# Optimization experiments

Measured on AMD Instinct MI355X. Metric: run time of the kernel, lower is better.

Reference implementation:

```python
import jax, jax.numpy as jnp
import numpy as np

D_MODEL = 768
D_STATE = 64
EXPAND = 2
D_INNER = EXPAND * D_MODEL
B, L = 2, 1024


def setup_inputs() -> dict:
    key = jax.random.key(0)
    ks = jax.random.split(key, 12)
    def xavier(k, shape):
        fan_in, fan_out = shape[0], shape[1]
        a = np.sqrt(6.0 / (fan_in + fan_out)).astype(np.float32)
        return jax.random.uniform(k, shape, jnp.float32, -a, a)
    x = jax.random.normal(ks[0], (B, L, D_MODEL), jnp.float32)
    W_in = xavier(ks[1], (D_MODEL, 2 * D_INNER))
    W_x = xavier(ks[2], (D_INNER, 2 * D_STATE + D_INNER))
    W_dt = xavier(ks[3], (D_STATE, D_INNER))
    b_dt = jax.random.uniform(ks[4], (D_INNER,), jnp.float32, -0.1, 0.1)
    A_log = jax.random.uniform(ks[5], (D_INNER, D_STATE), jnp.float32, -4.0, -1.0)
    Dp = 1.0 + 0.1 * jax.random.normal(ks[6], (D_INNER,), jnp.float32)
    W_out = xavier(ks[7], (D_INNER, D_MODEL))
    ln_g = jnp.ones((D_MODEL,), jnp.float32)
    ln_b = jnp.zeros((D_MODEL,), jnp.float32)
    return {"x": x, "W_in": W_in, "W_x": W_x, "W_dt": W_dt, "b_dt": b_dt,
            "A_log": A_log, "Dp": Dp, "W_out": W_out, "ln_g": ln_g, "ln_b": ln_b}


def _s6_forward(x, W_in, W_x, W_dt, b_dt, A_log, Dp, W_out, ln_g, ln_b):
    residual = x
    xr = x @ W_in                                    # (B,L,2*d_inner)
    xs, res = xr[..., :D_INNER], xr[..., D_INNER:]
    xs = jax.nn.silu(xs)
    # selective scan parameters
    x_dbl = xs @ W_x                                 # (B,L,2*d_state+d_inner)
    B_sel = x_dbl[..., :D_STATE]                     # (B,L,d_state)
    delta_in = x_dbl[..., D_STATE:2 * D_STATE]       # (B,L,d_state)
    C_sel = x_dbl[..., 2 * D_STATE:]                 # (B,L,d_inner)
    delta = jax.nn.softplus(delta_in @ W_dt + b_dt)  # (B,L,d_inner)
    delta = jnp.minimum(delta, 10.0)
    A = -jnp.exp(A_log.astype(jnp.float32))          # (d_inner,d_state)

    def step(h, inp):
        x_t, d_t, B_t, C_t = inp                     # (B,di) (B,di) (B,ds) (B,di)
        dA = jnp.exp(d_t[:, :, None] * A[None])      # (B,di,ds)
        dB = d_t[:, :, None] * B_t[:, None, :]       # (B,di,ds)
        h = dA * h + dB * x_t[:, :, None]
        y_t = C_t * jnp.sum(h, axis=-1)              # (B,di): sum(C[...,None]*h,-1)
        return h, y_t

    h0 = jnp.zeros((x.shape[0], D_INNER, D_STATE), xs.dtype)
    time_major = lambda a: jnp.swapaxes(a, 0, 1)
    _, ys = jax.lax.scan(step, h0, (time_major(xs), time_major(delta),
                                    time_major(B_sel), time_major(C_sel)))
    y = jnp.swapaxes(ys, 0, 1)                       # (B,L,d_inner)
    y = y + xs * Dp
    y = y * jax.nn.silu(res)
    out = y @ W_out + residual
    mu = jnp.mean(out, axis=-1, keepdims=True)
    var = jnp.var(out, axis=-1, keepdims=True)
    return (out - mu) * jax.lax.rsqrt(var + 1e-5) * ln_g + ln_b


def reference(x, W_in, W_x, W_dt, b_dt, A_log, Dp, W_out, ln_g, ln_b):
    return _s6_forward(x, W_in, W_x, W_dt, b_dt, A_log, Dp, W_out, ln_g, ln_b)
```

## Files before the change

### kernel.cpp

```cpp
#include <hip/hip_runtime.h>

typedef __bf16 bf16x8 __attribute__((ext_vector_type(8)));
typedef short short8 __attribute__((ext_vector_type(8)));
typedef float f32x4 __attribute__((ext_vector_type(4)));
typedef float f32x2 __attribute__((ext_vector_type(2)));
typedef unsigned short ushort_t;

__device__ __forceinline__ ushort_t f2bf(float f) {
  union { float f; unsigned u; } v; v.f = f;
  unsigned r = v.u + 0x7fffu + ((v.u >> 16) & 1u);
  return (ushort_t)(r >> 16);
}

__device__ __forceinline__ void g2lds16(const void* g, void* l) {
  __builtin_amdgcn_global_load_lds(
      (const __attribute__((address_space(1))) void*)g,
      (__attribute__((address_space(3))) void*)l, 16, 0, 0);
}

__device__ __forceinline__ float rlane(float v, int l) {
  return __int_as_float(__builtin_amdgcn_readlane(__float_as_int(v), l));
}

__device__ __forceinline__ float fexp2(float x) {
#if __has_builtin(__builtin_amdgcn_exp2f)
  return __builtin_amdgcn_exp2f(x);
#else
  return exp2f(x);
#endif
}

__device__ __forceinline__ f32x2 pk_fma(f32x2 a, f32x2 b, f32x2 c) {
#if __has_builtin(__builtin_elementwise_fma)
  return __builtin_elementwise_fma(a, b, c);
#else
  return (f32x2){fmaf(a.x, b.x, c.x), fmaf(a.y, b.y, c.y)};
#endif
}

template<int CTRL>
__device__ __forceinline__ float dpp_step(float x) {
  int t = __builtin_amdgcn_update_dpp(0, __float_as_int(x), CTRL, 0xf, 0xf, false);
  return x + __int_as_float(t);
}
__device__ __forceinline__ float wave_sum64(float v) {
  v = dpp_step<0x111>(v);
  v = dpp_step<0x112>(v);
  v = dpp_step<0x114>(v);
  v = dpp_step<0x118>(v);
  v = dpp_step<0x142>(v);
  v = dpp_step<0x143>(v);
  return v;
}
__device__ __forceinline__ float row_sum16(float v) {
  v = dpp_step<0x111>(v);
  v = dpp_step<0x112>(v);
  v = dpp_step<0x114>(v);
  v = dpp_step<0x118>(v);
  return v;
}

__global__ __launch_bounds__(256)
void prep_kernel(const float* __restrict__ x, ushort_t* __restrict__ xbf,
                 const float* __restrict__ W_in, ushort_t* __restrict__ WinT,
                 const float* __restrict__ W_x, ushort_t* __restrict__ WxT,
                 const float* __restrict__ W_out, ushort_t* __restrict__ WoutT) {
  __shared__ float tile[32][33];
  const int r = blockIdx.x, tid = threadIdx.x;
  if (r < 1536) {
    int i = (r * 256 + tid) * 4;
    float4 v = *(const float4*)(x + i);
    union { ushort_t u[4]; uint2 v2; } o;
    o.u[0] = f2bf(v.x); o.u[1] = f2bf(v.y); o.u[2] = f2bf(v.z); o.u[3] = f2bf(v.w);
    *(uint2*)(xbf + i) = o.v2;
    return;
  }
  const float* W; ushort_t* Wt; int K, N, bx, by;
  if (r < 3840)      { int rr = r - 1536; W = W_in;  Wt = WinT;  K = 768;  N = 3072; bx = rr % 96; by = rr / 96; }
  else if (r < 6336) { int rr = r - 3840; W = W_x;   Wt = WxT;   K = 1536; N = 1664; bx = rr % 52; by = rr / 52; }
  else               { int rr = r - 6336; W = W_out; Wt = WoutT; K = 1536; N = 768;  bx = rr % 24; by = rr / 24; }
  const int n0 = bx * 32, k0 = by * 32;
  const int tx = tid & 31, ty = tid >> 5;
#pragma unroll
  for (int rr = 0; rr < 32; rr += 8)
    tile[ty + rr][tx] = W[(size_t)(k0 + ty + rr) * N + n0 + tx];
  __syncthreads();
#pragma unroll
  for (int rr = 0; rr < 32; rr += 8)
    Wt[(size_t)(n0 + ty + rr) * K + k0 + tx] = f2bf(tile[tx][ty + rr]);
}

template<int MODE>
__global__ __launch_bounds__(256)
void gemm_bf16(const ushort_t* __restrict__ A, const ushort_t* __restrict__ Bt,
               const int K, const int lda, const int ldb,
               float* __restrict__ out0, ushort_t* __restrict__ out1,
               float* __restrict__ out2, const float* __restrict__ resid) {
  __shared__ __align__(16) ushort_t Asl[128 * 32];
  __shared__ __align__(16) ushort_t Bsl[64 * 32];
  const int tid = threadIdx.x;
  const int lane = tid & 63;
  const int wid = tid >> 6;
  const int wm = wid >> 1, wn = wid & 1;
  const int lr = lane & 15, lk = lane >> 4;
  const int bm = blockIdx.y, bn = blockIdx.x;
  if (MODE == 2) {
    const int z = blockIdx.z;
    A += z * 768;
    Bt += z * 768;
    out0 += (size_t)z * 2048 * 768;
  }
  const ushort_t* Ab = A + (size_t)bm * 128 * lda;
  const ushort_t* Bb = Bt + (size_t)bn * 64 * ldb;

  f32x4 acc[4][2];
#pragma unroll
  for (int i = 0; i < 4; ++i)
#pragma unroll
    for (int j = 0; j < 2; ++j) acc[i][j] = (f32x4){0.f, 0.f, 0.f, 0.f};

  for (int k0 = 0; k0 < K; k0 += 32) {
#pragma unroll
    for (int it = 0; it < 2; ++it) {
      const int cb = ((it << 2) + wid) << 6;
      const int ch = cb + lane;
      const int row = ch >> 2;
      const int c8 = (ch & 3) << 3;
      g2lds16(Ab + (size_t)row * lda + k0 + c8, Asl + (size_t)cb * 8);
    }
    {
      const int cb = wid << 6;
      const int ch = cb + lane;
      const int row = ch >> 2;
      const int c8 = (ch & 3) << 3;
      g2lds16(Bb + (size_t)row * ldb + k0 + c8, Bsl + (size_t)cb * 8);
    }
    __syncthreads();
    short8 av[4], bv[2];
#pragma unroll
    for (int i = 0; i < 4; ++i)
      av[i] = *(const short8*)(Asl + ((wm * 64 + i * 16 + lr) * 32 + lk * 8));
#pragma unroll
    for (int j = 0; j < 2; ++j)
      bv[j] = *(const short8*)(Bsl + ((wn * 32 + j * 16 + lr) * 32 + lk * 8));
#pragma unroll
    for (int i = 0; i < 4; ++i)
#pragma unroll
      for (int j = 0; j < 2; ++j)
        acc[i][j] = __builtin_amdgcn_mfma_f32_16x16x32_bf16(
            __builtin_bit_cast(bf16x8, av[i]), __builtin_bit_cast(bf16x8, bv[j]),
            acc[i][j], 0, 0, 0);
    __syncthreads();
  }

  const int mb = bm * 128 + wm * 64 + (lane >> 4) * 4;
  const int nb = bn * 64 + wn * 32 + (lane & 15);
#pragma unroll
  for (int i = 0; i < 4; ++i) {
#pragma unroll
    for (int j = 0; j < 2; ++j) {
      const int n = nb + j * 16;
#pragma unroll
      for (int r = 0; r < 4; ++r) {
        const int m = mb + i * 16 + r;
        float v = acc[i][j][r];
        if (MODE == 0) {
          float sv = v / (1.f + __expf(-v));
          if (n < 1536) {
            out0[(size_t)m * 1536 + n] = sv;
            out1[(size_t)m * 1536 + n] = f2bf(sv);
          } else {
            out2[(size_t)m * 1536 + (n - 1536)] = sv;
          }
        } else if (MODE == 1) {
          out0[(size_t)m * 1664 + n] = v;
        } else {
          out0[(size_t)m * 768 + n] = v;
        }
      }
    }
  }
}

__global__ __launch_bounds__(256)
void dt_gemm(const float* __restrict__ xdbl, const float* __restrict__ Wdt,
             const float* __restrict__ bdt, float* __restrict__ delta) {
  __shared__ float Wl[64][256];
  __shared__ float Xl[32][64];
  const int tid = threadIdx.x;
  const int n0 = blockIdx.x << 8;
  const int m0 = blockIdx.y << 5;
  for (int i = tid; i < 64 * 256; i += 256) {
    int k = i >> 8, nn = i & 255;
    Wl[k][nn] = Wdt[(size_t)k * 1536 + n0 + nn];
  }
  for (int i = tid; i < 32 * 64; i += 256) {
    int mm = i >> 6, k = i & 63;
    Xl[mm][k] = xdbl[(size_t)(m0 + mm) * 1664 + 64 + k];
  }
  __syncthreads();
  float bv = bdt[n0 + tid];
  for (int mm = 0; mm < 32; ++mm) {
    float acc = bv;
#pragma unroll
    for (int k = 0; k < 64; ++k) acc = fmaf(Xl[mm][k], Wl[k][tid], acc);
    float sp = fmaxf(acc, 0.f) + log1pf(__expf(-fabsf(acc)));
    delta[(size_t)(m0 + mm) * 1536 + n0 + tid] = fminf(sp, 10.f);
  }
}


__global__ __launch_bounds__(256)
void scan_pass1(const float* __restrict__ xdbl, const float* __restrict__ delta,
                const float* __restrict__ xs, const float* __restrict__ A_log,
                float* __restrict__ Qb, float* __restrict__ Dsum) {
  __shared__ __align__(16) ushort_t Btl[32 * 64 * 2];
  __shared__ __align__(16) f32x4 ddl[32 * 16];
  const int tid = threadIdx.x;
  const int lane = tid & 63;
  const int wid = tid >> 6;
  const int i16 = lane & 15;
  const int ch = wid * 4 + (lane >> 4);
  const int seg = blockIdx.x, b = blockIdx.z;
  const int d0 = blockIdx.y * 16;
  const int d = d0 + ch;
  const int t0 = seg << 6;
  const size_t r0 = (size_t)b * 1024;

#pragma unroll
  for (int i = 0; i < 2; ++i) {
    int q = i * 256 + tid;
    int t2 = q >> 4, s0 = (q & 15) << 2;
    const float* rowE = xdbl + (r0 + t0 + 2 * t2) * 1664 + s0;
    float4 ve = *(const float4*)rowE;
    float4 vo = *(const float4*)(rowE + 1664);
    uint4 u;
    u.x = f2bf(ve.x) | ((unsigned)f2bf(vo.x) << 16);
    u.y = f2bf(ve.y) | ((unsigned)f2bf(vo.y) << 16);
    u.z = f2bf(ve.z) | ((unsigned)f2bf(vo.z) << 16);
    u.w = f2bf(ve.w) | ((unsigned)f2bf(vo.w) << 16);
    *(uint4*)&Btl[(t2 * 64 + s0) * 2] = u;
  }
  const int t2w = lane >> 1;
  float dtg[4];
#pragma unroll
  for (int c = 0; c < 4; ++c) {
    int dc = d0 + wid * 4 + c;
    dtg[c] = delta[(r0 + t0 + lane) * 1536 + dc];
    float dxg = dtg[c] * xs[(r0 + t0 + lane) * 1536 + dc];
    int cx = (wid * 4 + c) ^ (t2w & 15);
    float* slot = (float*)&ddl[t2w * 16 + cx] + (lane & 1) * 2;
    *(f32x2*)slot = (f32x2){dtg[c], dxg};
  }
  float ds0 = rlane(wave_sum64(dtg[0]), 63);
  float ds1 = rlane(wave_sum64(dtg[1]), 63);
  float ds2 = rlane(wave_sum64(dtg[2]), 63);
  float ds3 = rlane(wave_sum64(dtg[3]), 63);
  if (lane == 0) {
    const size_t sb0 = (size_t)(b * 16 + seg) * 1536 + d0 + wid * 4;
    *(float4*)(Dsum + sb0) = make_float4(ds0, ds1, ds2, ds3);
  }

  float4 Av = *(const float4*)(A_log + (size_t)d * 64 + i16 * 4);
  const f32x2 A01 = {-__expf(Av.x) * 1.44269504f, -__expf(Av.y) * 1.44269504f};
  const f32x2 A23 = {-__expf(Av.z) * 1.44269504f, -__expf(Av.w) * 1.44269504f};

  __syncthreads();

  const char* ddb = (const char*)ddl;
  const char* Bb8 = (const char*)Btl + (i16 << 4);
  const int chb = ch << 4;
  f32x2 h01 = {0.f, 0.f}, h23 = {0.f, 0.f};
#pragma unroll
  for (int t2 = 0; t2 < 32; ++t2) {
    f32x4 dd = *(const f32x4*)(ddb + t2 * 256 + (chb ^ ((t2 & 15) << 4)));
    uint4 ub = *(const uint4*)(Bb8 + t2 * 256);
    f32x2 b01 = {__int_as_float(ub.x << 16), __int_as_float(ub.y << 16)};
    f32x2 b23 = {__int_as_float(ub.z << 16), __int_as_float(ub.w << 16)};
    f32x2 dt2 = {dd.x, dd.x}, dx2 = {dd.y, dd.y};
    f32x2 m01 = dt2 * A01, m23 = dt2 * A23;
    h01 = pk_fma((f32x2){fexp2(m01.x), fexp2(m01.y)}, h01, dx2 * b01);
    h23 = pk_fma((f32x2){fexp2(m23.x), fexp2(m23.y)}, h23, dx2 * b23);
    b01 = (f32x2){__int_as_float(ub.x & 0xFFFF0000u), __int_as_float(ub.y & 0xFFFF0000u)};
    b23 = (f32x2){__int_as_float(ub.z & 0xFFFF0000u), __int_as_float(ub.w & 0xFFFF0000u)};
    dt2 = (f32x2){dd.z, dd.z}; dx2 = (f32x2){dd.w, dd.w};
    m01 = dt2 * A01; m23 = dt2 * A23;
    h01 = pk_fma((f32x2){fexp2(m01.x), fexp2(m01.y)}, h01, dx2 * b01);
    h23 = pk_fma((f32x2){fexp2(m23.x), fexp2(m23.y)}, h23, dx2 * b23);
  }
  const size_t sb = (size_t)(b * 16 + seg) * 1536 + d;
  *(float4*)(Qb + sb * 64 + i16 * 4) = make_float4(h01.x, h01.y, h23.x, h23.y);
}

__global__ __launch_bounds__(256)
void scan_combine(float* __restrict__ Qb, const float* __restrict__ Dsum,
                  const float* __restrict__ A_log) {
  const int tid = threadIdx.x;
  const int lane = tid & 63;
  const int wave = blockIdx.x * 4 + (tid >> 6);
  const int bb = (wave >= 1536) ? 1 : 0;
  const int d = wave - bb * 1536;
  const float Aval2 = -__expf(A_log[(size_t)d * 64 + lane]) * 1.44269504f;
  float qv[16], Pv[16];
#pragma unroll
  for (int j = 0; j < 16; ++j) {
    const size_t sb = ((size_t)(bb * 16 + j) * 1536 + d);
    qv[j] = Qb[sb * 64 + lane];
    Pv[j] = fexp2(Aval2 * Dsum[sb]);
  }
  float h = 0.f;
#pragma unroll
  for (int j = 0; j < 16; ++j) {
    const size_t sb = ((size_t)(bb * 16 + j) * 1536 + d);
    Qb[sb * 64 + lane] = h;
    h = fmaf(Pv[j], h, qv[j]);
  }
}

__global__ __launch_bounds__(256)
void scan_pass2(const float* __restrict__ xdbl, const float* __restrict__ delta,
                const float* __restrict__ xs, const float* __restrict__ sres,
                const float* __restrict__ A_log, const float* __restrict__ Dp,
                const float* __restrict__ Qb, ushort_t* __restrict__ ybf) {
  __shared__ __align__(16) ushort_t Btl[32 * 64 * 2];
  __shared__ __align__(16) f32x4 ddl[32 * 16];
  __shared__ __align__(16) f32x2 ytl[32 * 16];
  const int tid = threadIdx.x;
  const int lane = tid & 63;
  const int wid = tid >> 6;
  const int i16 = lane & 15;
  const int ch = wid * 4 + (lane >> 4);
  const int seg = blockIdx.x, b = blockIdx.z;
  const int d0 = blockIdx.y * 16;
  const int d = d0 + ch;
  const int t0 = seg << 6;
  const size_t r0 = (size_t)b * 1024;

#pragma unroll
  for (int i = 0; i < 2; ++i) {
    int q = i * 256 + tid;
    int t2 = q >> 4, s0 = (q & 15) << 2;
    const float* rowE = xdbl + (r0 + t0 + 2 * t2) * 1664 + s0;
    float4 ve = *(const float4*)rowE;
    float4 vo = *(const float4*)(rowE + 1664);
    uint4 u;
    u.x = f2bf(ve.x) | ((unsigned)f2bf(vo.x) << 16);
    u.y = f2bf(ve.y) | ((unsigned)f2bf(vo.y) << 16);
    u.z = f2bf(ve.z) | ((unsigned)f2bf(vo.z) << 16);
    u.w = f2bf(ve.w) | ((unsigned)f2bf(vo.w) << 16);
    *(uint4*)&Btl[(t2 * 64 + s0) * 2] = u;
  }
  const int t2w = lane >> 1;
#pragma unroll
  for (int c = 0; c < 4; ++c) {
    int dc = d0 + wid * 4 + c;
    float dt = delta[(r0 + t0 + lane) * 1536 + dc];
    float dx = dt * xs[(r0 + t0 + lane) * 1536 + dc];
    int cx = (wid * 4 + c) ^ (t2w & 15);
    float* slot = (float*)&ddl[t2w * 16 + cx] + (lane & 1) * 2;
    *(f32x2*)slot = (f32x2){dt, dx};
  }

  float4 Av = *(const float4*)(A_log + (size_t)d * 64 + i16 * 4);
  const f32x2 A01 = {-__expf(Av.x) * 1.44269504f, -__expf(Av.y) * 1.44269504f};
  const f32x2 A23 = {-__expf(Av.z) * 1.44269504f, -__expf(Av.w) * 1.44269504f};
  const size_t sb = (size_t)(b * 16 + seg) * 1536 + d;
  float4 hq = *(const float4*)(Qb + sb * 64 + i16 * 4);
  f32x2 h01 = {hq.x, hq.y}, h23 = {hq.z, hq.w};

  __syncthreads();

  const char* ddb = (const char*)ddl;
  const char* Bb8 = (const char*)Btl + (i16 << 4);
  const int chb = ch << 4;
  const bool wlane = (i16 == 15);
#pragma unroll
  for (int t2 = 0; t2 < 32; ++t2) {
    f32x4 dd = *(const f32x4*)(ddb + t2 * 256 + (chb ^ ((t2 & 15) << 4)));
    uint4 ub = *(const uint4*)(Bb8 + t2 * 256);
    f32x2 b01 = {__int_as_float(ub.x << 16), __int_as_float(ub.y << 16)};
    f32x2 b23 = {__int_as_float(ub.z << 16), __int_as_float(ub.w << 16)};
    f32x2 dt2 = {dd.x, dd.x}, dx2 = {dd.y, dd.y};
    f32x2 m01 = dt2 * A01, m23 = dt2 * A23;
    h01 = pk_fma((f32x2){fexp2(m01.x), fexp2(m01.y)}, h01, dx2 * b01);
    h23 = pk_fma((f32x2){fexp2(m23.x), fexp2(m23.y)}, h23, dx2 * b23);
    f32x2 hsE = h01 + h23;
    float WE = row_sum16(hsE.x + hsE.y);
    b01 = (f32x2){__int_as_float(ub.x & 0xFFFF0000u), __int_as_float(ub.y & 0xFFFF0000u)};
    b23 = (f32x2){__int_as_float(ub.z & 0xFFFF0000u), __int_as_float(ub.w & 0xFFFF0000u)};
    dt2 = (f32x2){dd.z, dd.z}; dx2 = (f32x2){dd.w, dd.w};
    m01 = dt2 * A01; m23 = dt2 * A23;
    h01 = pk_fma((f32x2){fexp2(m01.x), fexp2(m01.y)}, h01, dx2 * b01);
    h23 = pk_fma((f32x2){fexp2(m23.x), fexp2(m23.y)}, h23, dx2 * b23);
    f32x2 hsO = h01 + h23;
    float WO = row_sum16(hsO.x + hsO.y);
    if (wlane) ytl[t2 * 16 + ch] = (f32x2){WE, WO};
  }
  __syncthreads();

  const int ch2 = tid & 15;
  const int tr = tid >> 4;
  const float dp2 = Dp[d0 + ch2];
  const float* ytf = (const float*)ytl;
#pragma unroll
  for (int r2 = 0; r2 < 4; ++r2) {
    const int t = tr + (r2 << 4);
    const size_t gi = r0 + t0 + t;
    float yv = ytf[(t >> 1) * 32 + ch2 * 2 + (t & 1)];
    float Ct = xdbl[gi * 1664 + 128 + d0 + ch2];
    float xt = xs[gi * 1536 + d0 + ch2];
    float rt = sres[gi * 1536 + d0 + ch2];
    ybf[gi * 1536 + d0 + ch2] = f2bf((Ct * yv + xt * dp2) * rt);
  }
}

__global__ __launch_bounds__(256)
void ln_kernel(const float* __restrict__ part, const float* __restrict__ x,
               const float* __restrict__ g, const float* __restrict__ be,
               float* __restrict__ outp) {
  const int row = blockIdx.x, tid = threadIdx.x;
  const size_t ro = (size_t)row * 768;
  const float* p0 = part + ro;
  const float* p1 = part + 1572864 + ro;
  const float* xr = x + ro;
  float v0 = p0[tid] + p1[tid] + xr[tid];
  float v1 = p0[tid + 256] + p1[tid + 256] + xr[tid + 256];
  float v2 = p0[tid + 512] + p1[tid + 512] + xr[tid + 512];
  __shared__ float sb[4];
  const int wid = tid >> 6;
  float s = wave_sum64(v0 + v1 + v2);
  if ((tid & 63) == 63) sb[wid] = s;
  __syncthreads();
  float mu = (sb[0] + sb[1] + sb[2] + sb[3]) * (1.f / 768.f);
  __syncthreads();
  float d0 = v0 - mu, d1 = v1 - mu, d2 = v2 - mu;
  float q = wave_sum64(d0 * d0 + d1 * d1 + d2 * d2);
  if ((tid & 63) == 63) sb[wid] = q;
  __syncthreads();
  float var = (sb[0] + sb[1] + sb[2] + sb[3]) * (1.f / 768.f);
  float inv = rsqrtf(var + 1e-5f);
  float* po = outp + ro;
  po[tid]       = d0 * inv * g[tid]       + be[tid];
  po[tid + 256] = d1 * inv * g[tid + 256] + be[tid + 256];
  po[tid + 512] = d2 * inv * g[tid + 512] + be[tid + 512];
}

extern "C" void kernel_launch(void* const* d_in, const int* in_sizes, int n_in,
                              void* d_out, int out_size, void* d_ws, size_t ws_size,
                              hipStream_t stream) {
  (void)in_sizes; (void)n_in; (void)out_size; (void)ws_size;
  const float* x     = (const float*)d_in[0];
  const float* W_in  = (const float*)d_in[1];
  const float* W_x   = (const float*)d_in[2];
  const float* W_dt  = (const float*)d_in[3];
  const float* b_dt  = (const float*)d_in[4];
  const float* A_log = (const float*)d_in[5];
  const float* Dp    = (const float*)d_in[6];
  const float* W_out = (const float*)d_in[7];
  const float* ln_g  = (const float*)d_in[8];
  const float* ln_b  = (const float*)d_in[9];
  float* out = (float*)d_out;
  char* ws = (char*)d_ws;

  ushort_t* xbf   = (ushort_t*)(ws + 0);
  ushort_t* WinT  = (ushort_t*)(ws + 3145728);
  ushort_t* WxT   = (ushort_t*)(ws + 7864320);
  ushort_t* WoutT = (ushort_t*)(ws + 12976128);
  float*    xs_f  = (float*)   (ws + 15335424);
  ushort_t* xs_bf = (ushort_t*)(ws + 27918336);
  float*    sresp = (float*)   (ws + 34209792);
  float*    xdbl  = (float*)   (ws + 46792704);
  float*    dlt   = (float*)   (ws + 60424192);
  ushort_t* ybf   = (ushort_t*)(ws + 73007104);
  float*    Qbuf  = (float*)   (ws + 0);
  float*    Dsum  = (float*)   (ws + 12582912);
  float*    part  = (float*)   (ws + 15335424);

  prep_kernel<<<7488, 256, 0, stream>>>(x, xbf, W_in, WinT, W_x, WxT, W_out, WoutT);

  gemm_bf16<0><<<dim3(48, 16), 256, 0, stream>>>(xbf, WinT, 768, 768, 768,
                                                 xs_f, xs_bf, sresp, nullptr);
  gemm_bf16<1><<<dim3(26, 16), 256, 0, stream>>>(xs_bf, WxT, 1536, 1536, 1536,
                                                 xdbl, nullptr, nullptr, nullptr);
  dt_gemm<<<dim3(6, 64), 256, 0, stream>>>(xdbl, W_dt, b_dt, dlt);

  scan_pass1<<<dim3(16, 96, 2), 256, 0, stream>>>(xdbl, dlt, xs_f, A_log, Qbuf, Dsum);
  scan_combine<<<768, 256, 0, stream>>>(Qbuf, Dsum, A_log);
  scan_pass2<<<dim3(16, 96, 2), 256, 0, stream>>>(xdbl, dlt, xs_f, sresp, A_log, Dp, Qbuf, ybf);

  gemm_bf16<2><<<dim3(12, 16, 2), 256, 0, stream>>>(ybf, WoutT, 768, 1536, 1536,
                                                    part, nullptr, nullptr, nullptr);
  ln_kernel<<<2048, 256, 0, stream>>>(part, x, ln_g, ln_b, out);
}
```

Before: 207.3 us.

## Fuse dt projection into scan passes via MFMA and shrink GEMM tiles to 64x64

The separate dt_gemm kernel and its delta buffer are removed. Each scan pass now recomputes the delta projection for its 64-step, 16-channel tile with bf16 MFMA, applies softplus and clamp in registers, and reduces delta sums through LDS. The bf16 GEMMs drop from 128x64 to 64x64 tiles, doubling the grid to improve occupancy and CU coverage. This trades one kernel launch and the delta write/read for the projection being computed twice, once per pass, and lowers the delta projection precision from fp32 to bf16.

```diff
diff --git a/kernel.cpp b/kernel.cpp
--- a/kernel.cpp
+++ b/kernel.cpp
@@ -16,10 +16,6 @@
   __builtin_amdgcn_global_load_lds(
       (const __attribute__((address_space(1))) void*)g,
       (__attribute__((address_space(3))) void*)l, 16, 0, 0);
-}
-
-__device__ __forceinline__ float rlane(float v, int l) {
-  return __int_as_float(__builtin_amdgcn_readlane(__float_as_int(v), l));
 }
 
 __device__ __forceinline__ float fexp2(float x) {
@@ -92,11 +88,11 @@
 
 template<int MODE>
 __global__ __launch_bounds__(256)
-void gemm_bf16(const ushort_t* __restrict__ A, const ushort_t* __restrict__ Bt,
-               const int K, const int lda, const int ldb,
-               float* __restrict__ out0, ushort_t* __restrict__ out1,
-               float* __restrict__ out2, const float* __restrict__ resid) {
-  __shared__ __align__(16) ushort_t Asl[128 * 32];
+void gemm64(const ushort_t* __restrict__ A, const ushort_t* __restrict__ Bt,
+            const int K, const int lda, const int ldb,
+            float* __restrict__ out0, ushort_t* __restrict__ out1,
+            float* __restrict__ out2) {
+  __shared__ __align__(16) ushort_t Asl[64 * 32];
   __shared__ __align__(16) ushort_t Bsl[64 * 32];
   const int tid = threadIdx.x;
   const int lane = tid & 63;
@@ -104,47 +100,42 @@
   const int wm = wid >> 1, wn = wid & 1;
   const int lr = lane & 15, lk = lane >> 4;
   const int bm = blockIdx.y, bn = blockIdx.x;
+  const ushort_t* Ab;
+  const ushort_t* Bb;
+  float* o0 = out0;
   if (MODE == 2) {
     const int z = blockIdx.z;
-    A += z * 768;
-    Bt += z * 768;
-    out0 += (size_t)z * 2048 * 768;
-  }
-  const ushort_t* Ab = A + (size_t)bm * 128 * lda;
-  const ushort_t* Bb = Bt + (size_t)bn * 64 * ldb;
-
-  f32x4 acc[4][2];
-#pragma unroll
-  for (int i = 0; i < 4; ++i)
+    Ab = A + z * 768 + (size_t)bm * 64 * lda;
+    Bb = Bt + z * 768 + (size_t)bn * 64 * ldb;
+    o0 = out0 + (size_t)z * 2048 * 768;
+  } else {
+    Ab = A + (size_t)bm * 64 * lda;
+    Bb = Bt + (size_t)bn * 64 * ldb;
+  }
+
+  f32x4 acc[2][2];
+#pragma unroll
+  for (int i = 0; i < 2; ++i)
 #pragma unroll
     for (int j = 0; j < 2; ++j) acc[i][j] = (f32x4){0.f, 0.f, 0.f, 0.f};
 
   for (int k0 = 0; k0 < K; k0 += 32) {
-#pragma unroll
-    for (int it = 0; it < 2; ++it) {
-      const int cb = ((it << 2) + wid) << 6;
-      const int ch = cb + lane;
-      const int row = ch >> 2;
-      const int c8 = (ch & 3) << 3;
-      g2lds16(Ab + (size_t)row * lda + k0 + c8, Asl + (size_t)cb * 8);
-    }
-    {
-      const int cb = wid << 6;
-      const int ch = cb + lane;
-      const int row = ch >> 2;
-      const int c8 = (ch & 3) << 3;
-      g2lds16(Bb + (size_t)row * ldb + k0 + c8, Bsl + (size_t)cb * 8);
-    }
+    const int cb = wid << 6;
+    const int ch = cb + lane;
+    const int row = ch >> 2;
+    const int c8 = (ch & 3) << 3;
+    g2lds16(Ab + (size_t)row * lda + k0 + c8, Asl + (size_t)cb * 8);
+    g2lds16(Bb + (size_t)row * ldb + k0 + c8, Bsl + (size_t)cb * 8);
     __syncthreads();
-    short8 av[4], bv[2];
-#pragma unroll
-    for (int i = 0; i < 4; ++i)
-      av[i] = *(const short8*)(Asl + ((wm * 64 + i * 16 + lr) * 32 + lk * 8));
+    short8 av[2], bv[2];
+#pragma unroll
+    for (int i = 0; i < 2; ++i)
+      av[i] = *(const short8*)(Asl + ((wm * 32 + i * 16 + lr) * 32 + lk * 8));
 #pragma unroll
     for (int j = 0; j < 2; ++j)
       bv[j] = *(const short8*)(Bsl + ((wn * 32 + j * 16 + lr) * 32 + lk * 8));
 #pragma unroll
-    for (int i = 0; i < 4; ++i)
+    for (int i = 0; i < 2; ++i)
 #pragma unroll
       for (int j = 0; j < 2; ++j)
         acc[i][j] = __builtin_amdgcn_mfma_f32_16x16x32_bf16(
@@ -153,10 +144,10 @@
     __syncthreads();
   }
 
-  const int mb = bm * 128 + wm * 64 + (lane >> 4) * 4;
-  const int nb = bn * 64 + wn * 32 + (lane & 15);
-#pragma unroll
-  for (int i = 0; i < 4; ++i) {
+  const int mb = bm * 64 + wm * 32 + (lane >> 4) * 4;
+  const int nb = bn * 64 + wn * 32 + lr;
+#pragma unroll
+  for (int i = 0; i < 2; ++i) {
 #pragma unroll
     for (int j = 0; j < 2; ++j) {
       const int n = nb + j * 16;
@@ -175,7 +166,7 @@
         } else if (MODE == 1) {
           out0[(size_t)m * 1664 + n] = v;
         } else {
-          out0[(size_t)m * 768 + n] = v;
+          o0[(size_t)m * 768 + n] = v;
         }
       }
     }
@@ -183,50 +174,81 @@
 }
 
 __global__ __launch_bounds__(256)
-void dt_gemm(const float* __restrict__ xdbl, const float* __restrict__ Wdt,
-             const float* __restrict__ bdt, float* __restrict__ delta) {
-  __shared__ float Wl[64][256];
-  __shared__ float Xl[32][64];
-  const int tid = threadIdx.x;
-  const int n0 = blockIdx.x << 8;
-  const int m0 = blockIdx.y << 5;
-  for (int i = tid; i < 64 * 256; i += 256) {
-    int k = i >> 8, nn = i & 255;
-    Wl[k][nn] = Wdt[(size_t)k * 1536 + n0 + nn];
-  }
-  for (int i = tid; i < 32 * 64; i += 256) {
-    int mm = i >> 6, k = i & 63;
-    Xl[mm][k] = xdbl[(size_t)(m0 + mm) * 1664 + 64 + k];
-  }
-  __syncthreads();
-  float bv = bdt[n0 + tid];
-  for (int mm = 0; mm < 32; ++mm) {
-    float acc = bv;
-#pragma unroll
-    for (int k = 0; k < 64; ++k) acc = fmaf(Xl[mm][k], Wl[k][tid], acc);
-    float sp = fmaxf(acc, 0.f) + log1pf(__expf(-fabsf(acc)));
-    delta[(size_t)(m0 + mm) * 1536 + n0 + tid] = fminf(sp, 10.f);
-  }
-}
-
-
-__global__ __launch_bounds__(256)
-void scan_pass1(const float* __restrict__ xdbl, const float* __restrict__ delta,
-                const float* __restrict__ xs, const float* __restrict__ A_log,
+void scan_pass1(const float* __restrict__ xdbl, const float* __restrict__ xs,
+                const float* __restrict__ W_dt, const float* __restrict__ b_dt,
+                const float* __restrict__ A_log,
                 float* __restrict__ Qb, float* __restrict__ Dsum) {
-  __shared__ __align__(16) ushort_t Btl[32 * 64 * 2];
-  __shared__ __align__(16) f32x4 ddl[32 * 16];
+  __shared__ __align__(16) char region[16384];
+  __shared__ float dsp[8][16];
+  ushort_t* Btl = (ushort_t*)region;
+  f32x4* ddl = (f32x4*)(region + 8192);
+  ushort_t* DinF = (ushort_t*)region;
+  ushort_t* WdtS = (ushort_t*)(region + 8704);
   const int tid = threadIdx.x;
   const int lane = tid & 63;
   const int wid = tid >> 6;
   const int i16 = lane & 15;
-  const int ch = wid * 4 + (lane >> 4);
+  const int lk = lane >> 4;
+  const int ch = wid * 4 + lk;
   const int seg = blockIdx.x, b = blockIdx.z;
   const int d0 = blockIdx.y * 16;
   const int d = d0 + ch;
   const int t0 = seg << 6;
   const size_t r0 = (size_t)b * 1024;
 
+#pragma unroll
+  for (int i = 0; i < 4; ++i) {
+    int q = i * 256 + tid;
+    int t = q >> 4, k4 = (q & 15) << 2;
+    float4 v = *(const float4*)(xdbl + (r0 + t0 + t) * 1664 + 64 + k4);
+    union { ushort_t u[4]; uint2 p; } o;
+    o.u[0] = f2bf(v.x); o.u[1] = f2bf(v.y); o.u[2] = f2bf(v.z); o.u[3] = f2bf(v.w);
+    *(uint2*)&DinF[t * 68 + k4] = o.p;
+  }
+  {
+    int k = tid >> 2, c4 = (tid & 3) << 2;
+    float4 w = *(const float4*)(W_dt + (size_t)k * 1536 + d0 + c4);
+    WdtS[(c4 + 0) * 68 + k] = f2bf(w.x);
+    WdtS[(c4 + 1) * 68 + k] = f2bf(w.y);
+    WdtS[(c4 + 2) * 68 + k] = f2bf(w.z);
+    WdtS[(c4 + 3) * 68 + k] = f2bf(w.w);
+  }
+  const float bbias = b_dt[d0 + i16];
+  float4 Av = *(const float4*)(A_log + (size_t)d * 64 + i16 * 4);
+  const f32x2 A01 = {-__expf(Av.x) * 1.44269504f, -__expf(Av.y) * 1.44269504f};
+  const f32x2 A23 = {-__expf(Av.z) * 1.44269504f, -__expf(Av.w) * 1.44269504f};
+  __syncthreads();
+
+  f32x4 dacc = (f32x4){0.f, 0.f, 0.f, 0.f};
+  {
+    short8 a0 = *(const short8*)&DinF[(wid * 16 + i16) * 68 + lk * 8];
+    short8 b0 = *(const short8*)&WdtS[i16 * 68 + lk * 8];
+    dacc = __builtin_amdgcn_mfma_f32_16x16x32_bf16(
+        __builtin_bit_cast(bf16x8, a0), __builtin_bit_cast(bf16x8, b0), dacc, 0, 0, 0);
+    short8 a1 = *(const short8*)&DinF[(wid * 16 + i16) * 68 + 32 + lk * 8];
+    short8 b1 = *(const short8*)&WdtS[i16 * 68 + 32 + lk * 8];
+    dacc = __builtin_amdgcn_mfma_f32_16x16x32_bf16(
+        __builtin_bit_cast(bf16x8, a1), __builtin_bit_cast(bf16x8, b1), dacc, 0, 0, 0);
+  }
+  float sp[4], dx[4];
+  const int tbase = wid * 16 + lk * 4;
+#pragma unroll
+  for (int r = 0; r < 4; ++r) {
+    float a = dacc[r] + bbias;
+    float s = fmaxf(a, 0.f) + log1pf(__expf(-fabsf(a)));
+    sp[r] = fminf(s, 10.f);
+    dx[r] = sp[r] * xs[(r0 + t0 + tbase + r) * 1536 + d0 + i16];
+  }
+  float part = (sp[0] + sp[1]) + (sp[2] + sp[3]);
+  part += __int_as_float(__builtin_amdgcn_ds_swizzle(__float_as_int(part), 0x401F));
+  __syncthreads();
+  if ((lane & 16) == 0) dsp[wid * 2 + (lane >> 5)][i16] = part;
+  {
+    const int t2a = tbase >> 1;
+    ddl[t2a * 16 + (i16 ^ (t2a & 15))] = (f32x4){sp[0], dx[0], sp[1], dx[1]};
+    const int t2b = t2a + 1;
+    ddl[t2b * 16 + (i16 ^ (t2b & 15))] = (f32x4){sp[2], dx[2], sp[3], dx[3]};
+  }
 #pragma unroll
   for (int i = 0; i < 2; ++i) {
     int q = i * 256 + tid;
@@ -241,31 +263,12 @@
     u.w = f2bf(ve.w) | ((unsigned)f2bf(vo.w) << 16);
     *(uint4*)&Btl[(t2 * 64 + s0) * 2] = u;
   }
-  const int t2w = lane >> 1;
-  float dtg[4];
-#pragma unroll
-  for (int c = 0; c < 4; ++c) {
-    int dc = d0 + wid * 4 + c;
-    dtg[c] = delta[(r0 + t0 + lane) * 1536 + dc];
-    float dxg = dtg[c] * xs[(r0 + t0 + lane) * 1536 + dc];
-    int cx = (wid * 4 + c) ^ (t2w & 15);
-    float* slot = (float*)&ddl[t2w * 16 + cx] + (lane & 1) * 2;
-    *(f32x2*)slot = (f32x2){dtg[c], dxg};
-  }
-  float ds0 = rlane(wave_sum64(dtg[0]), 63);
-  float ds1 = rlane(wave_sum64(dtg[1]), 63);
-  float ds2 = rlane(wave_sum64(dtg[2]), 63);
-  float ds3 = rlane(wave_sum64(dtg[3]), 63);
-  if (lane == 0) {
-    const size_t sb0 = (size_t)(b * 16 + seg) * 1536 + d0 + wid * 4;
-    *(float4*)(Dsum + sb0) = make_float4(ds0, ds1, ds2, ds3);
-  }
-
-  float4 Av = *(const float4*)(A_log + (size_t)d * 64 + i16 * 4);
-  const f32x2 A01 = {-__expf(Av.x) * 1.44269504f, -__expf(Av.y) * 1.44269504f};
-  const f32x2 A23 = {-__expf(Av.z) * 1.44269504f, -__expf(Av.w) * 1.44269504f};
-
-  __syncthreads();
+  __syncthreads();
+  if (tid < 16) {
+    float s = ((dsp[0][tid] + dsp[1][tid]) + (dsp[2][tid] + dsp[3][tid])) +
+              ((dsp[4][tid] + dsp[5][tid]) + (dsp[6][tid] + dsp[7][tid]));
+    Dsum[(size_t)(b * 16 + seg) * 1536 + d0 + tid] = s;
+  }
 
   const char* ddb = (const char*)ddl;
   const char* Bb8 = (const char*)Btl + (i16 << 4);
@@ -288,8 +291,8 @@
     h01 = pk_fma((f32x2){fexp2(m01.x), fexp2(m01.y)}, h01, dx2 * b01);
     h23 = pk_fma((f32x2){fexp2(m23.x), fexp2(m23.y)}, h23, dx2 * b23);
   }
-  const size_t sb = (size_t)(b * 16 + seg) * 1536 + d;
-  *(float4*)(Qb + sb * 64 + i16 * 4) = make_float4(h01.x, h01.y, h23.x, h23.y);
+  const size_t sbq = (size_t)(b * 16 + seg) * 1536 + d;
+  *(float4*)(Qb + sbq * 64 + i16 * 4) = make_float4(h01.x, h01.y, h23.x, h23.y);
 }
 
 __global__ __launch_bounds__(256)
@@ -318,24 +321,82 @@
 }
 
 __global__ __launch_bounds__(256)
-void scan_pass2(const float* __restrict__ xdbl, const float* __restrict__ delta,
-                const float* __restrict__ xs, const float* __restrict__ sres,
-                const float* __restrict__ A_log, const float* __restrict__ Dp,
-                const float* __restrict__ Qb, ushort_t* __restrict__ ybf) {
-  __shared__ __align__(16) ushort_t Btl[32 * 64 * 2];
-  __shared__ __align__(16) f32x4 ddl[32 * 16];
+void scan_pass2(const float* __restrict__ xdbl, const float* __restrict__ xs,
+                const float* __restrict__ sres, const float* __restrict__ W_dt,
+                const float* __restrict__ b_dt, const float* __restrict__ A_log,
+                const float* __restrict__ Dp, const float* __restrict__ Qb,
+                ushort_t* __restrict__ ybf) {
+  __shared__ __align__(16) char region[16384];
   __shared__ __align__(16) f32x2 ytl[32 * 16];
+  ushort_t* Btl = (ushort_t*)region;
+  f32x4* ddl = (f32x4*)(region + 8192);
+  ushort_t* DinF = (ushort_t*)region;
+  ushort_t* WdtS = (ushort_t*)(region + 8704);
   const int tid = threadIdx.x;
   const int lane = tid & 63;
   const int wid = tid >> 6;
   const int i16 = lane & 15;
-  const int ch = wid * 4 + (lane >> 4);
+  const int lk = lane >> 4;
+  const int ch = wid * 4 + lk;
   const int seg = blockIdx.x, b = blockIdx.z;
   const int d0 = blockIdx.y * 16;
   const int d = d0 + ch;
   const int t0 = seg << 6;
   const size_t r0 = (size_t)b * 1024;
 
+#pragma unroll
+  for (int i = 0; i < 4; ++i) {
+    int q = i * 256 + tid;
+    int t = q >> 4, k4 = (q & 15) << 2;
+    float4 v = *(const float4*)(xdbl + (r0 + t0 + t) * 1664 + 64 + k4);
+    union { ushort_t u[4]; uint2 p; } o;
+    o.u[0] = f2bf(v.x); o.u[1] = f2bf(v.y); o.u[2] = f2bf(v.z); o.u[3] = f2bf(v.w);
+    *(uint2*)&DinF[t * 68 + k4] = o.p;
+  }
+  {
+    int k = tid >> 2, c4 = (tid & 3) << 2;
+    float4 w = *(const float4*)(W_dt + (size_t)k * 1536 + d0 + c4);
+    WdtS[(c4 + 0) * 68 + k] = f2bf(w.x);
+    WdtS[(c4 + 1) * 68 + k] = f2bf(w.y);
+    WdtS[(c4 + 2) * 68 + k] = f2bf(w.z);
+    WdtS[(c4 + 3) * 68 + k] = f2bf(w.w);
+  }
+  const float bbias = b_dt[d0 + i16];
+  float4 Av = *(const float4*)(A_log + (size_t)d * 64 + i16 * 4);
+  const f32x2 A01 = {-__expf(Av.x) * 1.44269504f, -__expf(Av.y) * 1.44269504f};
+  const f32x2 A23 = {-__expf(Av.z) * 1.44269504f, -__expf(Av.w) * 1.44269504f};
+  const size_t sbq = (size_t)(b * 16 + seg) * 1536 + d;
+  float4 hq = *(const float4*)(Qb + sbq * 64 + i16 * 4);
+  f32x2 h01 = {hq.x, hq.y}, h23 = {hq.z, hq.w};
+  __syncthreads();
+
+  f32x4 dacc = (f32x4){0.f, 0.f, 0.f, 0.f};
+  {
+    short8 a0 = *(const short8*)&DinF[(wid * 16 + i16) * 68 + lk * 8];
+    short8 b0 = *(const short8*)&WdtS[i16 * 68 + lk * 8];
+    dacc = __builtin_amdgcn_mfma_f32_16x16x32_bf16(
+        __builtin_bit_cast(bf16x8, a0), __builtin_bit_cast(bf16x8, b0), dacc, 0, 0, 0);
+    short8 a1 = *(const short8*)&DinF[(wid * 16 + i16) * 68 + 32 + lk * 8];
+    short8 b1 = *(const short8*)&WdtS[i16 * 68 + 32 + lk * 8];
+    dacc = __builtin_amdgcn_mfma_f32_16x16x32_bf16(
+        __builtin_bit_cast(bf16x8, a1), __builtin_bit_cast(bf16x8, b1), dacc, 0, 0, 0);
+  }
+  float sp[4], dx[4];
+  const int tbase = wid * 16 + lk * 4;
+#pragma unroll
+  for (int r = 0; r < 4; ++r) {
+    float a = dacc[r] + bbias;
+    float s = fmaxf(a, 0.f) + log1pf(__expf(-fabsf(a)));
+    sp[r] = fminf(s, 10.f);
+    dx[r] = sp[r] * xs[(r0 + t0 + tbase + r) * 1536 + d0 + i16];
+  }
+  __syncthreads();
+  {
+    const int t2a = tbase >> 1;
+    ddl[t2a * 16 + (i16 ^ (t2a & 15))] = (f32x4){sp[0], dx[0], sp[1], dx[1]};
+    const int t2b = t2a + 1;
+    ddl[t2b * 16 + (i16 ^ (t2b & 15))] = (f32x4){sp[2], dx[2], sp[3], dx[3]};
+  }
 #pragma unroll
   for (int i = 0; i < 2; ++i) {
     int q = i * 256 + tid;
@@ -350,24 +411,6 @@
     u.w = f2bf(ve.w) | ((unsigned)f2bf(vo.w) << 16);
     *(uint4*)&Btl[(t2 * 64 + s0) * 2] = u;
   }
-  const int t2w = lane >> 1;
-#pragma unroll
-  for (int c = 0; c < 4; ++c) {
-    int dc = d0 + wid * 4 + c;
-    float dt = delta[(r0 + t0 + lane) * 1536 + dc];
-    float dx = dt * xs[(r0 + t0 + lane) * 1536 + dc];
-    int cx = (wid * 4 + c) ^ (t2w & 15);
-    float* slot = (float*)&ddl[t2w * 16 + cx] + (lane & 1) * 2;
-    *(f32x2*)slot = (f32x2){dt, dx};
-  }
-
-  float4 Av = *(const float4*)(A_log + (size_t)d * 64 + i16 * 4);
-  const f32x2 A01 = {-__expf(Av.x) * 1.44269504f, -__expf(Av.y) * 1.44269504f};
-  const f32x2 A23 = {-__expf(Av.z) * 1.44269504f, -__expf(Av.w) * 1.44269504f};
-  const size_t sb = (size_t)(b * 16 + seg) * 1536 + d;
-  float4 hq = *(const float4*)(Qb + sb * 64 + i16 * 4);
-  f32x2 h01 = {hq.x, hq.y}, h23 = {hq.z, hq.w};
-
   __syncthreads();
 
   const char* ddb = (const char*)ddl;
@@ -470,7 +513,6 @@
   ushort_t* xs_bf = (ushort_t*)(ws + 27918336);
   float*    sresp = (float*)   (ws + 34209792);
   float*    xdbl  = (float*)   (ws + 46792704);
-  float*    dlt   = (float*)   (ws + 60424192);
   ushort_t* ybf   = (ushort_t*)(ws + 73007104);
   float*    Qbuf  = (float*)   (ws + 0);
   float*    Dsum  = (float*)   (ws + 12582912);
@@ -478,17 +520,18 @@
 
   prep_kernel<<<7488, 256, 0, stream>>>(x, xbf, W_in, WinT, W_x, WxT, W_out, WoutT);
 
-  gemm_bf16<0><<<dim3(48, 16), 256, 0, stream>>>(xbf, WinT, 768, 768, 768,
-                                                 xs_f, xs_bf, sresp, nullptr);
-  gemm_bf16<1><<<dim3(26, 16), 256, 0, stream>>>(xs_bf, WxT, 1536, 1536, 1536,
-                                                 xdbl, nullptr, nullptr, nullptr);
-  dt_gemm<<<dim3(6, 64), 256, 0, stream>>>(xdbl, W_dt, b_dt, dlt);
-
-  scan_pass1<<<dim3(16, 96, 2), 256, 0, stream>>>(xdbl, dlt, xs_f, A_log, Qbuf, Dsum);
+  gemm64<0><<<dim3(48, 32), 256, 0, stream>>>(xbf, WinT, 768, 768, 768,
+                                              xs_f, xs_bf, sresp);
+  gemm64<1><<<dim3(26, 32), 256, 0, stream>>>(xs_bf, WxT, 1536, 1536, 1536,
+                                              xdbl, nullptr, nullptr);
+
+  scan_pass1<<<dim3(16, 96, 2), 256, 0, stream>>>(xdbl, xs_f, W_dt, b_dt, A_log,
+                                                  Qbuf, Dsum);
   scan_combine<<<768, 256, 0, stream>>>(Qbuf, Dsum, A_log);
-  scan_pass2<<<dim3(16, 96, 2), 256, 0, stream>>>(xdbl, dlt, xs_f, sresp, A_log, Dp, Qbuf, ybf);
-
-  gemm_bf16<2><<<dim3(12, 16, 2), 256, 0, stream>>>(ybf, WoutT, 768, 1536, 1536,
-                                                    part, nullptr, nullptr, nullptr);
+  scan_pass2<<<dim3(16, 96, 2), 256, 0, stream>>>(xdbl, xs_f, sresp, W_dt, b_dt,
+                                                  A_log, Dp, Qbuf, ybf);
+
+  gemm64<2><<<dim3(12, 32, 2), 256, 0, stream>>>(ybf, WoutT, 768, 1536, 1536,
+                                                 part, nullptr, nullptr);
   ln_kernel<<<2048, 256, 0, stream>>>(part, x, ln_g, ln_b, out);
 }
```

Result: faster. 195.3 us (-5.8%).
